# Optimization experiments

Hardware: AMD Instinct MI355X
Metric: run time of the kernel (lower is better)

## Reference

```python
import jax, jax.numpy as jnp
import numpy as np

BS, NX = 4, 4096
SD, NPAR, H, L, K = 2, 5, 128, 6, 16
DT = 0.1
EPS = 1e-5


def swish(x):
    return x * jax.nn.sigmoid(x)


def _gather(a, idx):
    # a: [bs, nx, F], idx: [bs, nx, k] -> [bs, nx, k, F]
    bs, nx, k = idx.shape
    flat = jnp.take_along_axis(a, idx.reshape(bs, nx * k)[:, :, None], axis=1)
    return flat.reshape(bs, nx, k, a.shape[-1])


def _knn_idx(pos, k):
    # pos: [bs, nx, sd] -> indices of k nearest neighbors (self excluded), [bs, nx, k]
    sq = jnp.sum(pos * pos, axis=-1)
    d2 = sq[:, :, None] + sq[:, None, :] - 2.0 * jnp.einsum('bnd,bmd->bnm', pos, pos)
    n = pos.shape[1]
    d2 = d2.at[:, jnp.arange(n), jnp.arange(n)].set(1e10)  # loop=False
    return jax.lax.top_k(-d2, k)[1]


def _instance_norm(x):
    # PyG InstanceNorm (affine=False): normalize per graph per channel over nodes
    m = jnp.mean(x, axis=1, keepdims=True)
    v = jnp.mean((x - m) ** 2, axis=1, keepdims=True)
    return (x - m) * jax.lax.rsqrt(v + EPS)


def _forward(inputs, case_params, grid, emb_w1, emb_b1, emb_w2, emb_b2,
             mw1, mb1, mw2, mb2, uw1, ub1, uw2, ub2, ow1, ob1, ow2, ob2):
    u = inputs[..., :1]  # var_id=0 slice (c==1 here)
    # per-batch, per-dim min-max normalization of grid -> pos in [0,1]
    gmin = jnp.min(grid, axis=1, keepdims=True)
    gmax = jnp.max(grid, axis=1, keepdims=True)
    pos = (grid - gmin) / (gmax - gmin)
    idx = _knn_idx(pos, K)  # [bs, nx, K]: neighbors j of each target i
    params = case_params

    f = swish(jnp.concatenate([u, pos, params], -1) @ emb_w1 + emb_b1)
    f = swish(f @ emb_w2 + emb_b2)

    u_j = _gather(u, idx)
    pos_j = _gather(pos, idx)
    du = u[:, :, None, :] - u_j       # u_i - u_j,   [bs,nx,K,1]
    dpos = pos[:, :, None, :] - pos_j  # pos_i - pos_j, [bs,nx,K,sd]
    var_i = jnp.broadcast_to(params[:, :, None, :], (BS, NX, K, NPAR))

    for l in range(L):
        f_j = _gather(f, idx)
        f_i = jnp.broadcast_to(f[:, :, None, :], f_j.shape)
        m = jnp.concatenate([f_i, f_j, du, dpos, var_i], -1)  # [bs,nx,K,2H+1+sd+npar]
        m = swish(m @ mw1[l] + mb1[l])
        m = swish(m @ mw2[l] + mb2[l])
        agg = jnp.mean(m, axis=2)  # mean aggregation over K incoming edges
        up = swish(jnp.concatenate([f, agg, params], -1) @ uw1[l] + ub1[l])
        up = swish(up @ uw2[l] + ub2[l])
        f = _instance_norm(f + up)  # residual (in==out) then InstanceNorm

    diff = swish(f @ ow1 + ob1) @ ow2 + ob2
    return u + DT * diff  # [bs, nx, 1]


def setup_inputs():
    key = jax.random.key(0)
    ks = jax.random.split(key, 16)
    s = 0.05
    d = {}
    d['inputs'] = jax.random.normal(ks[0], (BS, NX, 1), jnp.float32)
    d['case_params'] = jax.random.uniform(ks[1], (BS, NX, NPAR), dtype=jnp.float32)
    d['mask'] = jnp.ones((BS, NX, 1), jnp.float32)
    d['grid'] = jax.random.uniform(ks[2], (BS, NX, SD), dtype=jnp.float32)
    d['emb_w1'] = jax.random.normal(ks[3], (1 + SD + NPAR, H), jnp.float32) * s
    d['emb_b1'] = jnp.zeros((H,), jnp.float32)
    d['emb_w2'] = jax.random.normal(ks[4], (H, H), jnp.float32) * s
    d['emb_b2'] = jnp.zeros((H,), jnp.float32)
    d['mw1'] = jax.random.normal(ks[5], (L, 2 * H + 1 + SD + NPAR, H), jnp.float32) * s
    d['mb1'] = jnp.zeros((L, H), jnp.float32)
    d['mw2'] = jax.random.normal(ks[6], (L, H, H), jnp.float32) * s
    d['mb2'] = jnp.zeros((L, H), jnp.float32)
    d['uw1'] = jax.random.normal(ks[7], (L, 2 * H + NPAR, H), jnp.float32) * s
    d['ub1'] = jnp.zeros((L, H), jnp.float32)
    d['uw2'] = jax.random.normal(ks[8], (L, H, H), jnp.float32) * s
    d['ub2'] = jnp.zeros((L, H), jnp.float32)
    d['ow1'] = jax.random.normal(ks[9], (H, H // 2), jnp.float32) * s
    d['ob1'] = jnp.zeros((H // 2,), jnp.float32)
    d['ow2'] = jax.random.normal(ks[10], (H // 2, 1), jnp.float32) * s
    d['ob2'] = jnp.zeros((1,), jnp.float32)
    return d


def reference(inputs, case_params, mask, grid, emb_w1, emb_b1, emb_w2, emb_b2,
              mw1, mb1, mw2, mb2, uw1, ub1, uw2, ub2, ow1, ob1, ow2, ob2):
    del mask  # unused by the original forward math
    return _forward(inputs, case_params, grid, emb_w1, emb_b1, emb_w2, emb_b2,
                    mw1, mb1, mw2, mb2, uw1, ub1, uw2, ub2, ow1, ob1, ow2, ob2)
```

## Files before the change

kernel.cpp:

```cpp
#include <hip/hip_runtime.h>
#include <math.h>

#define BSZ 4
#define NXN 4096
#define NPARP 5
#define HD 128
#define NLAY 6
#define KNN 16
#define DTC 0.1f
#define EPSC 1e-5f
#define NN (BSZ * NXN)
#define NPB 8
#define EPB 128

typedef __attribute__((ext_vector_type(8))) short short8;
typedef __attribute__((ext_vector_type(4))) float f32x4;

#define XR(r) (((r) & 7) << 4)

#define OFF_E   0
#define OFF_AU  32768
#define OFF_HU  40960
#define OFF_DU  45056
#define OFF_DPX 45568
#define OFF_DPY 46080
#define OFF_VAR 46592
#define SMEMB   46848

__device__ __forceinline__ float swishf(float x) {
    return x / (1.0f + __expf(-x));
}

__device__ __forceinline__ unsigned short f2bf(float x) {
    union { float f; unsigned u; } v; v.f = x;
    unsigned r = v.u + 0x7fffu + ((v.u >> 16) & 1u);
    return (unsigned short)(r >> 16);
}
__device__ __forceinline__ unsigned short trh(float x) {
    union { float f; unsigned u; } v; v.f = x;
    return (unsigned short)(v.u >> 16);
}

__global__ void kminmax(const float* __restrict__ grid, float* __restrict__ gmm) {
    int b = blockIdx.x;
    int t = threadIdx.x;
    float mnx = 1e30f, mxx = -1e30f, mny = 1e30f, mxy = -1e30f;
    for (int n = t; n < NXN; n += 256) {
        float x = grid[(b * NXN + n) * 2 + 0];
        float y = grid[(b * NXN + n) * 2 + 1];
        mnx = fminf(mnx, x); mxx = fmaxf(mxx, x);
        mny = fminf(mny, y); mxy = fmaxf(mxy, y);
    }
    __shared__ float s[4][256];
    s[0][t] = mnx; s[1][t] = mxx; s[2][t] = mny; s[3][t] = mxy;
    __syncthreads();
    for (int off = 128; off > 0; off >>= 1) {
        if (t < off) {
            s[0][t] = fminf(s[0][t], s[0][t + off]);
            s[1][t] = fmaxf(s[1][t], s[1][t + off]);
            s[2][t] = fminf(s[2][t], s[2][t + off]);
            s[3][t] = fmaxf(s[3][t], s[3][t + off]);
        }
        __syncthreads();
    }
    if (t == 0) {
        gmm[b * 4 + 0] = s[0][0];
        gmm[b * 4 + 1] = s[1][0];
        gmm[b * 4 + 2] = s[2][0];
        gmm[b * 4 + 3] = s[3][0];
    }
}

__global__ void kpos(const float* __restrict__ grid, const float* __restrict__ gmm,
                     float* __restrict__ pos, float* __restrict__ sq) {
    int g = blockIdx.x * 256 + threadIdx.x;
    if (g >= NN) return;
    int b = g >> 12;
    float gx = grid[g * 2], gy = grid[g * 2 + 1];
    float px = (gx - gmm[b * 4 + 0]) / (gmm[b * 4 + 1] - gmm[b * 4 + 0]);
    float py = (gy - gmm[b * 4 + 2]) / (gmm[b * 4 + 3] - gmm[b * 4 + 2]);
    pos[g * 2] = px; pos[g * 2 + 1] = py;
    sq[g] = __fadd_rn(__fmul_rn(px, px), __fmul_rn(py, py));
}

__global__ __launch_bounds__(256) void kknnC(const float* __restrict__ pos,
                                             const float* __restrict__ sq,
                                             int* __restrict__ idxw) {
    __shared__ float2 sxy[1024];
    __shared__ float ssq[1024];
    int blk = blockIdx.x;
    int b = blk >> 10;
    int t = threadIdx.x;
    int lane = t & 63, w = t >> 6;
    int i = (blk & 1023) * 4 + w;
    float2 pi = *(const float2*)&pos[(b * NXN + i) * 2];
    float sqi = sq[b * NXN + i];
    float pk[64];
    float g[4];
#pragma unroll
    for (int c = 0; c < 4; ++c) {
        __syncthreads();
        for (int n = t; n < 1024; n += 256) {
            int j = b * NXN + c * 1024 + n;
            sxy[n] = *(const float2*)&pos[j * 2];
            ssq[n] = sq[j];
        }
        __syncthreads();
        float gc = 1e38f;
#pragma unroll
        for (int tt = 0; tt < 16; ++tt) {
            int n = tt * 64 + lane;
            float2 pj = sxy[n];
            float dot = fmaf(pi.x, pj.x, pi.y * pj.y);
            float d2 = (sqi + ssq[n]) - 2.0f * dot;
            d2 = (c * 1024 + n == i) ? 1e38f : d2;
            pk[c * 16 + tt] = d2;
            gc = fminf(gc, d2);
        }
        g[c] = gc;
    }
    int obase = (b * NXN + i) * KNN;
#pragma unroll 1
    for (int r = 0; r < KNN; ++r) {
        float m = fminf(fminf(g[0], g[1]), fminf(g[2], g[3]));
        float gm = m;
#pragma unroll
        for (int off = 1; off < 64; off <<= 1)
            gm = fminf(gm, __shfl_xor(gm, off));
        if (m == gm) {
            int jt = 0;
            if (g[0] == gm) {
                float ng = 1e38f;
#pragma unroll
                for (int tt = 0; tt < 16; ++tt) {
                    bool hit = (pk[tt] == gm);
                    jt = hit ? tt : jt;
                    pk[tt] = hit ? 1e38f : pk[tt];
                    ng = fminf(ng, pk[tt]);
                }
                g[0] = ng;
            }
            if (g[1] == gm) {
                float ng = 1e38f;
#pragma unroll
                for (int tt = 16; tt < 32; ++tt) {
                    bool hit = (pk[tt] == gm);
                    jt = hit ? tt : jt;
                    pk[tt] = hit ? 1e38f : pk[tt];
                    ng = fminf(ng, pk[tt]);
                }
                g[1] = ng;
            }
            if (g[2] == gm) {
                float ng = 1e38f;
#pragma unroll
                for (int tt = 32; tt < 48; ++tt) {
                    bool hit = (pk[tt] == gm);
                    jt = hit ? tt : jt;
                    pk[tt] = hit ? 1e38f : pk[tt];
                    ng = fminf(ng, pk[tt]);
                }
                g[2] = ng;
            }
            if (g[3] == gm) {
                float ng = 1e38f;
#pragma unroll
                for (int tt = 48; tt < 64; ++tt) {
                    bool hit = (pk[tt] == gm);
                    jt = hit ? tt : jt;
                    pk[tt] = hit ? 1e38f : pk[tt];
                    ng = fminf(ng, pk[tt]);
                }
                g[3] = ng;
            }
            idxw[obase + r] = ((jt >> 4) << 10) + ((jt & 15) << 6) + lane;
        }
    }
}

__global__ void kpack(const float* __restrict__ src, unsigned short* __restrict__ dst,
                      int K, int KB, int nmat) {
    int g = blockIdx.x * 256 + threadIdx.x;
    int per = KB * 1024;
    if (g >= nmat * per) return;
    int mat = g / per, rem = g % per;
    int kb = rem >> 10, r2 = rem & 1023;
    int n = r2 >> 3, j = r2 & 7;
    int k = kb * 8 + j;
    float v = (k < K) ? src[(mat * K + k) * HD + n] : 0.0f;
    dst[g] = f2bf(v);
}

__global__ __launch_bounds__(128) void kembed(const float* __restrict__ inputs,
                                              const float* __restrict__ pos,
                                              const float* __restrict__ params,
                                              const float* __restrict__ w1,
                                              const float* __restrict__ b1,
                                              const float* __restrict__ w2,
                                              const float* __restrict__ b2,
                                              float* __restrict__ f,
                                              unsigned short* __restrict__ fh) {
    __shared__ __align__(16) float sh[HD];
    int t = threadIdx.x;
    int g = blockIdx.x;
    float rw1[8];
#pragma unroll
    for (int k = 0; k < 8; k++) rw1[k] = w1[k * HD + t];
    float u = inputs[g];
    float px = pos[g * 2], py = pos[g * 2 + 1];
    float a = b1[t] + u * rw1[0] + px * rw1[1] + py * rw1[2];
#pragma unroll
    for (int j = 0; j < NPARP; j++) a += params[g * NPARP + j] * rw1[3 + j];
    sh[t] = swishf(a);
    __syncthreads();
    float a2 = b2[t];
    for (int k = 0; k < HD; k += 4) {
        float4 s4 = *(const float4*)&sh[k];
        a2 = fmaf(s4.x, w2[(k + 0) * HD + t], a2);
        a2 = fmaf(s4.y, w2[(k + 1) * HD + t], a2);
        a2 = fmaf(s4.z, w2[(k + 2) * HD + t], a2);
        a2 = fmaf(s4.w, w2[(k + 3) * HD + t], a2);
    }
    float fv = swishf(a2);
    f[g * HD + t] = fv;
    fh[g * HD + t] = trh(fv);
}

__global__ __launch_bounds__(256, 3) void kmsg4(
    const float* __restrict__ f, const unsigned short* __restrict__ fh,
    float* __restrict__ fnew,
    const float* __restrict__ inputs, const float* __restrict__ pos,
    const float* __restrict__ params, const int* __restrict__ idxw,
    const unsigned short* __restrict__ W1p, const float* __restrict__ W1r,
    const float* __restrict__ B1,
    const unsigned short* __restrict__ W2p, const float* __restrict__ B2,
    const unsigned short* __restrict__ U1p, const float* __restrict__ U1r,
    const float* __restrict__ UB1,
    const unsigned short* __restrict__ U2p, const float* __restrict__ UB2) {
    __shared__ __align__(16) char sm[SMEMB];
    int tid = threadIdx.x;
    int lane = tid & 63, w = tid >> 6;
    int l15 = lane & 15, l4 = lane >> 4;
    int bn0 = blockIdx.x * NPB;
    int base = bn0 & ~(NXN - 1);
    int r0 = w * 32;
    int c0 = w * 32 + l15, c1 = c0 + 16;
    float* sVAR = (float*)(sm + OFF_VAR);

    short8 bC0[4], bC1[4], bM10[4], bM11[4];
#pragma unroll
    for (int k = 0; k < 4; ++k) {
        bC0[k]  = *(const short8*)&W1p[((k * 4 + l4) * HD + c0) * 8];
        bC1[k]  = *(const short8*)&W1p[((k * 4 + l4) * HD + c1) * 8];
        bM10[k] = *(const short8*)&W1p[((16 + k * 4 + l4) * HD + c0) * 8];
        bM11[k] = *(const short8*)&W1p[((16 + k * 4 + l4) * HD + c1) * 8];
    }
    float vB1_0 = B1[c0], vB1_1 = B1[c1];
    float wdu0 = W1r[256 * HD + c0], wdx0 = W1r[257 * HD + c0], wdy0 = W1r[258 * HD + c0];
    float wdu1 = W1r[256 * HD + c1], wdx1 = W1r[257 * HD + c1], wdy1 = W1r[258 * HD + c1];
    float wv0[5], wv1[5];
#pragma unroll
    for (int j = 0; j < 5; ++j) {
        wv0[j] = W1r[(259 + j) * HD + c0];
        wv1[j] = W1r[(259 + j) * HD + c1];
    }
    float vB2_0 = B2[c0], vB2_1 = B2[c1];

    if (lane < 32) {
        int e = r0 + lane;
        int nd = e >> 4;
        int gj = idxw[(bn0 + nd) * KNN + (e & 15)];
        int gn = base + gj;
        ((float*)(sm + OFF_DU))[e]  = inputs[bn0 + nd] - inputs[gn];
        ((float*)(sm + OFF_DPX))[e] = pos[(bn0 + nd) * 2]     - pos[gn * 2];
        ((float*)(sm + OFF_DPY))[e] = pos[(bn0 + nd) * 2 + 1] - pos[gn * 2 + 1];
    } else if (lane < 42) {
        int q = lane - 32;
        int nd = 2 * w + q / 5, j = q % 5;
        sVAR[nd * 8 + j] = params[(bn0 + nd) * NPARP + j];
    }
    {
        int r = 2 * w + (lane >> 5);
        int c4 = (lane & 31) * 4;
        uint2 v = *(const uint2*)&fh[(bn0 + r) * HD + c4];
        *(uint2*)(sm + OFF_AU + r * 512 + ((c4 * 2) ^ XR(r))) = v;
    }
    {
        int r = 8 + 2 * w + (lane >> 5);
        int cz = (lane & 31) * 16;
        uint4 z = {0, 0, 0, 0};
        *(uint4*)(sm + OFF_AU + r * 512 + cz) = z;
    }
    {
        int r = 8 + 2 * w + (lane >> 5);
        int cz = (lane & 31) * 8;
        uint2 z = {0, 0};
        *(uint2*)(sm + OFF_HU + r * 256 + cz) = z;
    }
    {
        int r = r0 + (lane >> 1), hf = lane & 1;
        int gj = idxw[(bn0 + (r >> 4)) * KNN + (r & 15)];
        const uint4* src = (const uint4*)&fh[(base + gj) * HD + hf * 64];
        char* drow = sm + OFF_E + r * 256;
#pragma unroll
        for (int jj = 0; jj < 8; ++jj) {
            uint4 p = src[jj];
            *(uint4*)(drow + ((hf * 128 + jj * 16) ^ XR(r))) = p;
        }
    }
    __syncthreads();

    f32x4 cm0 = {0.f, 0.f, 0.f, 0.f}, cm1 = {0.f, 0.f, 0.f, 0.f};
    {
        short8 afi[4];
#pragma unroll
        for (int k = 0; k < 4; ++k)
            afi[k] = *(short8*)(sm + OFF_AU + l15 * 512 + ((k * 64 + l4 * 16) ^ XR(l15)));
#pragma unroll
        for (int k = 0; k < 4; ++k) {
            cm0 = __builtin_amdgcn_mfma_f32_16x16x32_bf16(afi[k], bC0[k], cm0, 0, 0, 0);
            cm1 = __builtin_amdgcn_mfma_f32_16x16x32_bf16(afi[k], bC1[k], cm1, 0, 0, 0);
        }
    }
    if (l4 < 2) {
#pragma unroll
        for (int reg = 0; reg < 4; ++reg) {
            int nd = l4 * 4 + reg;
            float s0 = vB1_0, s1 = vB1_1;
#pragma unroll
            for (int j = 0; j < 5; ++j) {
                float vv = sVAR[nd * 8 + j];
                s0 = fmaf(vv, wv0[j], s0);
                s1 = fmaf(vv, wv1[j], s1);
            }
            cm0[reg] += s0; cm1[reg] += s1;
        }
    }

    short8 bM20[4], bM21[4];
#pragma unroll
    for (int k = 0; k < 4; ++k) {
        bM20[k] = *(const short8*)&W2p[((k * 4 + l4) * HD + c0) * 8];
        bM21[k] = *(const short8*)&W2p[((k * 4 + l4) * HD + c1) * 8];
    }

    short8 aC[4], aN[4];
#pragma unroll
    for (int k = 0; k < 4; ++k)
        aC[k] = *(short8*)(sm + OFF_E + l15 * 256 + ((k * 64 + l4 * 16) ^ XR(l15)));
#pragma unroll
    for (int m = 0; m < 8; ++m) {
        f32x4 h0 = {0.f, 0.f, 0.f, 0.f}, h1 = {0.f, 0.f, 0.f, 0.f};
#pragma unroll
        for (int k = 0; k < 4; ++k) {
            h0 = __builtin_amdgcn_mfma_f32_16x16x32_bf16(aC[k], bM10[k], h0, 0, 0, 0);
            h1 = __builtin_amdgcn_mfma_f32_16x16x32_bf16(aC[k], bM11[k], h1, 0, 0, 0);
        }
        if (m < 7) {
#pragma unroll
            for (int k = 0; k < 4; ++k)
                aN[k] = *(short8*)(sm + OFF_E + ((m + 1) * 16 + l15) * 256 +
                                   ((k * 64 + l4 * 16) ^ XR(l15)));
        }
        float com0 = __shfl(cm0[m & 3], ((m >> 2) << 4) | l15);
        float com1 = __shfl(cm1[m & 3], ((m >> 2) << 4) | l15);
        float4 duv = *(const float4*)(sm + OFF_DU  + (m * 16 + l4 * 4) * 4);
        float4 dxv = *(const float4*)(sm + OFF_DPX + (m * 16 + l4 * 4) * 4);
        float4 dyv = *(const float4*)(sm + OFF_DPY + (m * 16 + l4 * 4) * 4);
        __syncthreads();
#pragma unroll
        for (int reg = 0; reg < 4; ++reg) {
            int rr = m * 16 + l4 * 4 + reg;
            float d_u = ((const float*)&duv)[reg];
            float d_x = ((const float*)&dxv)[reg];
            float d_y = ((const float*)&dyv)[reg];
            float hv0 = h0[reg] + com0 + d_u * wdu0 + d_x * wdx0 + d_y * wdy0;
            *(unsigned short*)(sm + OFF_E + rr * 256 + ((c0 * 2) ^ XR(rr))) =
                trh(swishf(hv0));
            float hv1 = h1[reg] + com1 + d_u * wdu1 + d_x * wdx1 + d_y * wdy1;
            *(unsigned short*)(sm + OFF_E + rr * 256 + ((c1 * 2) ^ XR(rr))) =
                trh(swishf(hv1));
        }
        if (m < 7) {
#pragma unroll
            for (int k = 0; k < 4; ++k) aC[k] = aN[k];
        }
    }
    __syncthreads();

    short8 bU10[8], bU11[8];
#pragma unroll
    for (int k = 0; k < 8; ++k) {
        bU10[k] = *(const short8*)&U1p[((k * 4 + l4) * HD + c0) * 8];
        bU11[k] = *(const short8*)&U1p[((k * 4 + l4) * HD + c1) * 8];
    }
    float vUB1_0 = UB1[c0], vUB1_1 = UB1[c1];
    float uv0[5], uv1[5];
#pragma unroll
    for (int j = 0; j < 5; ++j) {
        uv0[j] = U1r[(256 + j) * HD + c0];
        uv1[j] = U1r[(256 + j) * HD + c1];
    }

#pragma unroll
    for (int m = 0; m < 8; ++m) {
        short8 hf4[4];
#pragma unroll
        for (int k = 0; k < 4; ++k)
            hf4[k] = *(short8*)(sm + OFF_E + (m * 16 + l15) * 256 +
                                ((k * 64 + l4 * 16) ^ XR(l15)));
        f32x4 s0 = {0.f, 0.f, 0.f, 0.f}, s1 = {0.f, 0.f, 0.f, 0.f};
#pragma unroll
        for (int k = 0; k < 4; ++k) {
            s0 = __builtin_amdgcn_mfma_f32_16x16x32_bf16(hf4[k], bM20[k], s0, 0, 0, 0);
            s1 = __builtin_amdgcn_mfma_f32_16x16x32_bf16(hf4[k], bM21[k], s1, 0, 0, 0);
        }
        float sum0 = swishf(s0[0] + vB2_0) + swishf(s0[1] + vB2_0)
                   + swishf(s0[2] + vB2_0) + swishf(s0[3] + vB2_0);
        float sum1 = swishf(s1[0] + vB2_1) + swishf(s1[1] + vB2_1)
                   + swishf(s1[2] + vB2_1) + swishf(s1[3] + vB2_1);
        sum0 += __shfl_xor(sum0, 16); sum0 += __shfl_xor(sum0, 32);
        sum1 += __shfl_xor(sum1, 16); sum1 += __shfl_xor(sum1, 32);
        if (lane < 16) {
            int ca = w * 32 + lane;
            *(unsigned short*)(sm + OFF_AU + m * 512 + ((256 + ca * 2) ^ XR(m))) =
                trh(sum0 * 0.0625f);
            *(unsigned short*)(sm + OFF_AU + m * 512 + ((256 + (ca + 16) * 2) ^ XR(m))) =
                trh(sum1 * 0.0625f);
        }
    }
    __syncthreads();

    short8 bU20[4], bU21[4];
#pragma unroll
    for (int k = 0; k < 4; ++k) {
        bU20[k] = *(const short8*)&U2p[((k * 4 + l4) * HD + c0) * 8];
        bU21[k] = *(const short8*)&U2p[((k * 4 + l4) * HD + c1) * 8];
    }
    float vUB2_0 = UB2[c0], vUB2_1 = UB2[c1];

    {
        short8 au[8];
#pragma unroll
        for (int k = 0; k < 8; ++k)
            au[k] = *(short8*)(sm + OFF_AU + l15 * 512 + ((k * 64 + l4 * 16) ^ XR(l15)));
        f32x4 u0 = {0.f, 0.f, 0.f, 0.f}, u1 = {0.f, 0.f, 0.f, 0.f};
#pragma unroll
        for (int k = 0; k < 8; ++k) {
            u0 = __builtin_amdgcn_mfma_f32_16x16x32_bf16(au[k], bU10[k], u0, 0, 0, 0);
            u1 = __builtin_amdgcn_mfma_f32_16x16x32_bf16(au[k], bU11[k], u1, 0, 0, 0);
        }
        if (l4 < 2) {
#pragma unroll
            for (int reg = 0; reg < 4; ++reg) {
                int nd = l4 * 4 + reg;
                float s0 = vUB1_0, s1 = vUB1_1;
#pragma unroll
                for (int j = 0; j < 5; ++j) {
                    float vv = sVAR[nd * 8 + j];
                    s0 = fmaf(vv, uv0[j], s0);
                    s1 = fmaf(vv, uv1[j], s1);
                }
                *(unsigned short*)(sm + OFF_HU + nd * 256 + ((c0 * 2) ^ XR(nd))) =
                    trh(swishf(u0[reg] + s0));
                *(unsigned short*)(sm + OFF_HU + nd * 256 + ((c1 * 2) ^ XR(nd))) =
                    trh(swishf(u1[reg] + s1));
            }
        }
    }
    __syncthreads();

    {
        short8 ah[4];
#pragma unroll
        for (int k = 0; k < 4; ++k)
            ah[k] = *(short8*)(sm + OFF_HU + l15 * 256 + ((k * 64 + l4 * 16) ^ XR(l15)));
        f32x4 o0 = {0.f, 0.f, 0.f, 0.f}, o1 = {0.f, 0.f, 0.f, 0.f};
#pragma unroll
        for (int k = 0; k < 4; ++k) {
            o0 = __builtin_amdgcn_mfma_f32_16x16x32_bf16(ah[k], bU20[k], o0, 0, 0, 0);
            o1 = __builtin_amdgcn_mfma_f32_16x16x32_bf16(ah[k], bU21[k], o1, 0, 0, 0);
        }
        if (l4 < 2) {
#pragma unroll
            for (int reg = 0; reg < 4; ++reg) {
                int nd = l4 * 4 + reg;
                int gi0 = (bn0 + nd) * HD + c0;
                fnew[gi0] = f[gi0] + swishf(o0[reg] + vUB2_0);
                int gi1 = (bn0 + nd) * HD + c1;
                fnew[gi1] = f[gi1] + swishf(o1[reg] + vUB2_1);
            }
        }
    }
}

__global__ __launch_bounds__(256) void kstats(const float* __restrict__ fnew,
                                              float* __restrict__ p1, float* __restrict__ p2) {
    int blk = blockIdx.x;
    int b = blk >> 5;
    int ch = blk & 31;
    int t = threadIdx.x;
    int c = t & 127;
    int half = t >> 7;
    int nbase = ch * 128;
    float s1 = 0.0f, s2 = 0.0f;
    for (int n = half; n < 128; n += 2) {
        float v = fnew[((b * NXN) + (nbase + n)) * HD + c];
        s1 += v; s2 += v * v;
    }
    __shared__ float r1[256], r2[256];
    r1[t] = s1; r2[t] = s2;
    __syncthreads();
    if (half == 0) {
        s1 += r1[t + 128]; s2 += r2[t + 128];
        p1[blk * HD + c] = s1;
        p2[blk * HD + c] = s2;
    }
}

__global__ void kfinal(const float* __restrict__ p1, const float* __restrict__ p2,
                       float* __restrict__ mean, float* __restrict__ inv) {
    int g = blockIdx.x * 256 + threadIdx.x;
    if (g >= BSZ * HD) return;
    int b = g >> 7;
    int c = g & 127;
    float s1 = 0.0f, s2 = 0.0f;
#pragma unroll
    for (int ch = 0; ch < 32; ch++) {
        s1 += p1[(b * 32 + ch) * HD + c];
        s2 += p2[(b * 32 + ch) * HD + c];
    }
    float m = s1 * (1.0f / NXN);
    float v = s2 * (1.0f / NXN) - m * m;
    mean[g] = m;
    inv[g] = rsqrtf(v + EPSC);
}

__global__ void kapply(const float* __restrict__ fnew,
                       const float* __restrict__ mean, const float* __restrict__ inv,
                       float* __restrict__ f, unsigned short* __restrict__ fh) {
    int g = blockIdx.x * 256 + threadIdx.x;
    int b = g >> 19;
    int c = g & 127;
    float fv = (fnew[g] - mean[b * HD + c]) * inv[b * HD + c];
    f[g] = fv;
    fh[g] = trh(fv);
}

__global__ __launch_bounds__(64) void khead(const float* __restrict__ f,
                                            const float* __restrict__ inputs,
                                            const float* __restrict__ ow1,
                                            const float* __restrict__ ob1,
                                            const float* __restrict__ ow2,
                                            const float* __restrict__ ob2,
                                            float* __restrict__ out) {
    int bn = blockIdx.x;
    int c = threadIdx.x;
    float a = ob1[c];
    for (int k = 0; k < HD; k++) a += f[bn * HD + k] * ow1[k * 64 + c];
    float v = swishf(a) * ow2[c];
#pragma unroll
    for (int off = 32; off > 0; off >>= 1) v += __shfl_down(v, off);
    if (c == 0) out[bn] = inputs[bn] + DTC * (v + ob2[0]);
}

extern "C" void kernel_launch(void* const* d_in, const int* in_sizes, int n_in,
                              void* d_out, int out_size, void* d_ws, size_t ws_size,
                              hipStream_t stream) {
    const float* inputs = (const float*)d_in[0];
    const float* params = (const float*)d_in[1];
    const float* grid   = (const float*)d_in[3];
    const float* emb_w1 = (const float*)d_in[4];
    const float* emb_b1 = (const float*)d_in[5];
    const float* emb_w2 = (const float*)d_in[6];
    const float* emb_b2 = (const float*)d_in[7];
    const float* mw1 = (const float*)d_in[8];
    const float* mb1 = (const float*)d_in[9];
    const float* mw2 = (const float*)d_in[10];
    const float* mb2 = (const float*)d_in[11];
    const float* uw1 = (const float*)d_in[12];
    const float* ub1 = (const float*)d_in[13];
    const float* uw2 = (const float*)d_in[14];
    const float* ub2 = (const float*)d_in[15];
    const float* ow1 = (const float*)d_in[16];
    const float* ob1 = (const float*)d_in[17];
    const float* ow2 = (const float*)d_in[18];
    const float* ob2 = (const float*)d_in[19];
    float* out = (float*)d_out;

    float* ws  = (float*)d_ws;
    float* pos = ws;
    float* sq  = pos + BSZ * NXN * 2;
    float* f   = sq + BSZ * NXN;
    float* fnew = f + BSZ * NXN * HD;
    float* p1   = fnew + BSZ * NXN * HD;
    float* p2   = p1 + BSZ * 32 * HD;
    float* meanw = p2 + BSZ * 32 * HD;
    float* invw  = meanw + BSZ * HD;
    float* gmm  = invw + BSZ * HD;
    int* idxw   = (int*)(gmm + 16);
    unsigned short* mw1p = (unsigned short*)(idxw + NN * KNN);
    unsigned short* mw2p = mw1p + 6 * 33 * 1024;
    unsigned short* uw1p = mw2p + 6 * 16 * 1024;
    unsigned short* uw2p = uw1p + 6 * 33 * 1024;
    unsigned short* fh   = uw2p + 6 * 16 * 1024;

    kminmax<<<BSZ, 256, 0, stream>>>(grid, gmm);
    kpos<<<NN / 256, 256, 0, stream>>>(grid, gmm, pos, sq);
    kknnC<<<BSZ * (NXN / 4), 256, 0, stream>>>(pos, sq, idxw);

    kpack<<<(6 * 33 * 1024 + 255) / 256, 256, 0, stream>>>(mw1, mw1p, 264, 33, 6);
    kpack<<<(6 * 16 * 1024 + 255) / 256, 256, 0, stream>>>(mw2, mw2p, 128, 16, 6);
    kpack<<<(6 * 33 * 1024 + 255) / 256, 256, 0, stream>>>(uw1, uw1p, 261, 33, 6);
    kpack<<<(6 * 16 * 1024 + 255) / 256, 256, 0, stream>>>(uw2, uw2p, 128, 16, 6);

    kembed<<<NN, 128, 0, stream>>>(inputs, pos, params,
                                   emb_w1, emb_b1, emb_w2, emb_b2, f, fh);
    for (int l = 0; l < NLAY; l++) {
        kmsg4<<<NN / NPB, 256, 0, stream>>>(f, fh, fnew, inputs, pos, params, idxw,
                                            mw1p + l * 33 * 1024, mw1 + l * 264 * HD, mb1 + l * HD,
                                            mw2p + l * 16 * 1024, mb2 + l * HD,
                                            uw1p + l * 33 * 1024, uw1 + l * 261 * HD, ub1 + l * HD,
                                            uw2p + l * 16 * 1024, ub2 + l * HD);
        kstats<<<BSZ * 32, 256, 0, stream>>>(fnew, p1, p2);
        kfinal<<<2, 256, 0, stream>>>(p1, p2, meanw, invw);
        kapply<<<(BSZ * NXN * HD) / 256, 256, 0, stream>>>(fnew, meanw, invw, f, fh);
    }
    khead<<<NN, 64, 0, stream>>>(f, inputs, ow1, ob1, ow2, ob2, out);
}
```

Before: 695.1 us.

## Fuse instance-norm statistics into message kernel via atomics and permute weight columns

Moves the per-graph channel sum and sum-of-squares into the message-passing kernel's epilogue, using wave shuffles and global atomicAdd, and drops the separate kstats and kfinal kernels. kapply now computes mean and inverse std directly from the accumulators, which are zeroed by a memset each layer. Packed weight columns are permuted so each lane owns adjacent channels, enabling 32-bit paired bf16 LDS stores and float2 global loads/stores. Swish uses a hardware reciprocal. This adds atomic contention and makes the float summation order nondeterministic.

After: 729.8 us. 5.0% more time.

```diff
diff --git a/kernel.cpp b/kernel.cpp
--- a/kernel.cpp
+++ b/kernel.cpp
@@ -28,7 +28,7 @@
 #define SMEMB   46848
 
 __device__ __forceinline__ float swishf(float x) {
-    return x / (1.0f + __expf(-x));
+    return x * __builtin_amdgcn_rcpf(1.0f + __expf(-x));
 }
 
 __device__ __forceinline__ unsigned short f2bf(float x) {
@@ -39,6 +39,10 @@
 __device__ __forceinline__ unsigned short trh(float x) {
     union { float f; unsigned u; } v; v.f = x;
     return (unsigned short)(v.u >> 16);
+}
+__device__ __forceinline__ unsigned trpk(float lo, float hi) {
+    union { float f; unsigned u; } a, b; a.f = lo; b.f = hi;
+    return (b.u & 0xFFFF0000u) | (a.u >> 16);
 }
 
 __global__ void kminmax(const float* __restrict__ grid, float* __restrict__ gmm) {
@@ -186,8 +190,9 @@
     int mat = g / per, rem = g % per;
     int kb = rem >> 10, r2 = rem & 1023;
     int n = r2 >> 3, j = r2 & 7;
+    int phys = (n & 96) | ((n & 15) << 1) | ((n >> 4) & 1);
     int k = kb * 8 + j;
-    float v = (k < K) ? src[(mat * K + k) * HD + n] : 0.0f;
+    float v = (k < K) ? src[(mat * K + k) * HD + phys] : 0.0f;
     dst[g] = f2bf(v);
 }
 
@@ -226,7 +231,7 @@
     fh[g * HD + t] = trh(fv);
 }
 
-__global__ __launch_bounds__(256, 3) void kmsg4(
+__global__ __launch_bounds__(256, 3) void kmsg5(
     const float* __restrict__ f, const unsigned short* __restrict__ fh,
     float* __restrict__ fnew,
     const float* __restrict__ inputs, const float* __restrict__ pos,
@@ -236,15 +241,18 @@
     const unsigned short* __restrict__ W2p, const float* __restrict__ B2,
     const unsigned short* __restrict__ U1p, const float* __restrict__ U1r,
     const float* __restrict__ UB1,
-    const unsigned short* __restrict__ U2p, const float* __restrict__ UB2) {
+    const unsigned short* __restrict__ U2p, const float* __restrict__ UB2,
+    float* __restrict__ p1, float* __restrict__ p2) {
     __shared__ __align__(16) char sm[SMEMB];
     int tid = threadIdx.x;
     int lane = tid & 63, w = tid >> 6;
     int l15 = lane & 15, l4 = lane >> 4;
     int bn0 = blockIdx.x * NPB;
     int base = bn0 & ~(NXN - 1);
+    int bb = bn0 >> 12;
     int r0 = w * 32;
     int c0 = w * 32 + l15, c1 = c0 + 16;
+    int pc0 = w * 32 + 2 * l15, pc1 = pc0 + 1;
     float* sVAR = (float*)(sm + OFF_VAR);
 
     short8 bC0[4], bC1[4], bM10[4], bM11[4];
@@ -255,16 +263,16 @@
         bM10[k] = *(const short8*)&W1p[((16 + k * 4 + l4) * HD + c0) * 8];
         bM11[k] = *(const short8*)&W1p[((16 + k * 4 + l4) * HD + c1) * 8];
     }
-    float vB1_0 = B1[c0], vB1_1 = B1[c1];
-    float wdu0 = W1r[256 * HD + c0], wdx0 = W1r[257 * HD + c0], wdy0 = W1r[258 * HD + c0];
-    float wdu1 = W1r[256 * HD + c1], wdx1 = W1r[257 * HD + c1], wdy1 = W1r[258 * HD + c1];
+    float vB1_0 = B1[pc0], vB1_1 = B1[pc1];
+    float wdu0 = W1r[256 * HD + pc0], wdx0 = W1r[257 * HD + pc0], wdy0 = W1r[258 * HD + pc0];
+    float wdu1 = W1r[256 * HD + pc1], wdx1 = W1r[257 * HD + pc1], wdy1 = W1r[258 * HD + pc1];
     float wv0[5], wv1[5];
 #pragma unroll
     for (int j = 0; j < 5; ++j) {
-        wv0[j] = W1r[(259 + j) * HD + c0];
-        wv1[j] = W1r[(259 + j) * HD + c1];
-    }
-    float vB2_0 = B2[c0], vB2_1 = B2[c1];
+        wv0[j] = W1r[(259 + j) * HD + pc0];
+        wv1[j] = W1r[(259 + j) * HD + pc1];
+    }
+    float vB2_0 = B2[pc0], vB2_1 = B2[pc1];
 
     if (lane < 32) {
         int e = r0 + lane;
@@ -375,11 +383,9 @@
             float d_x = ((const float*)&dxv)[reg];
             float d_y = ((const float*)&dyv)[reg];
             float hv0 = h0[reg] + com0 + d_u * wdu0 + d_x * wdx0 + d_y * wdy0;
-            *(unsigned short*)(sm + OFF_E + rr * 256 + ((c0 * 2) ^ XR(rr))) =
-                trh(swishf(hv0));
             float hv1 = h1[reg] + com1 + d_u * wdu1 + d_x * wdx1 + d_y * wdy1;
-            *(unsigned short*)(sm + OFF_E + rr * 256 + ((c1 * 2) ^ XR(rr))) =
-                trh(swishf(hv1));
+            *(unsigned*)(sm + OFF_E + rr * 256 + ((w * 64 + l15 * 4) ^ XR(rr))) =
+                trpk(swishf(hv0), swishf(hv1));
         }
         if (m < 7) {
 #pragma unroll
@@ -394,12 +400,12 @@
         bU10[k] = *(const short8*)&U1p[((k * 4 + l4) * HD + c0) * 8];
         bU11[k] = *(const short8*)&U1p[((k * 4 + l4) * HD + c1) * 8];
     }
-    float vUB1_0 = UB1[c0], vUB1_1 = UB1[c1];
+    float vUB1_0 = UB1[pc0], vUB1_1 = UB1[pc1];
     float uv0[5], uv1[5];
 #pragma unroll
     for (int j = 0; j < 5; ++j) {
-        uv0[j] = U1r[(256 + j) * HD + c0];
-        uv1[j] = U1r[(256 + j) * HD + c1];
+        uv0[j] = U1r[(256 + j) * HD + pc0];
+        uv1[j] = U1r[(256 + j) * HD + pc1];
     }
 
 #pragma unroll
@@ -422,11 +428,8 @@
         sum0 += __shfl_xor(sum0, 16); sum0 += __shfl_xor(sum0, 32);
         sum1 += __shfl_xor(sum1, 16); sum1 += __shfl_xor(sum1, 32);
         if (lane < 16) {
-            int ca = w * 32 + lane;
-            *(unsigned short*)(sm + OFF_AU + m * 512 + ((256 + ca * 2) ^ XR(m))) =
-                trh(sum0 * 0.0625f);
-            *(unsigned short*)(sm + OFF_AU + m * 512 + ((256 + (ca + 16) * 2) ^ XR(m))) =
-                trh(sum1 * 0.0625f);
+            *(unsigned*)(sm + OFF_AU + m * 512 + ((256 + w * 64 + lane * 4) ^ XR(m))) =
+                trpk(sum0 * 0.0625f, sum1 * 0.0625f);
         }
     }
     __syncthreads();
@@ -437,7 +440,7 @@
         bU20[k] = *(const short8*)&U2p[((k * 4 + l4) * HD + c0) * 8];
         bU21[k] = *(const short8*)&U2p[((k * 4 + l4) * HD + c1) * 8];
     }
-    float vUB2_0 = UB2[c0], vUB2_1 = UB2[c1];
+    float vUB2_0 = UB2[pc0], vUB2_1 = UB2[pc1];
 
     {
         short8 au[8];
@@ -461,10 +464,8 @@
                     s0 = fmaf(vv, uv0[j], s0);
                     s1 = fmaf(vv, uv1[j], s1);
                 }
-                *(unsigned short*)(sm + OFF_HU + nd * 256 + ((c0 * 2) ^ XR(nd))) =
-                    trh(swishf(u0[reg] + s0));
-                *(unsigned short*)(sm + OFF_HU + nd * 256 + ((c1 * 2) ^ XR(nd))) =
-                    trh(swishf(u1[reg] + s1));
+                *(unsigned*)(sm + OFF_HU + nd * 256 + ((w * 64 + l15 * 4) ^ XR(nd))) =
+                    trpk(swishf(u0[reg] + s0), swishf(u1[reg] + s1));
             }
         }
     }
@@ -481,68 +482,41 @@
             o0 = __builtin_amdgcn_mfma_f32_16x16x32_bf16(ah[k], bU20[k], o0, 0, 0, 0);
             o1 = __builtin_amdgcn_mfma_f32_16x16x32_bf16(ah[k], bU21[k], o1, 0, 0, 0);
         }
+        float a1_0 = 0.f, a2_0 = 0.f, a1_1 = 0.f, a2_1 = 0.f;
         if (l4 < 2) {
 #pragma unroll
             for (int reg = 0; reg < 4; ++reg) {
                 int nd = l4 * 4 + reg;
-                int gi0 = (bn0 + nd) * HD + c0;
-                fnew[gi0] = f[gi0] + swishf(o0[reg] + vUB2_0);
-                int gi1 = (bn0 + nd) * HD + c1;
-                fnew[gi1] = f[gi1] + swishf(o1[reg] + vUB2_1);
+                int gi = (bn0 + nd) * HD + pc0;
+                float2 fv = *(const float2*)&f[gi];
+                float v0 = fv.x + swishf(o0[reg] + vUB2_0);
+                float v1 = fv.y + swishf(o1[reg] + vUB2_1);
+                float2 st = {v0, v1};
+                *(float2*)&fnew[gi] = st;
+                a1_0 += v0; a2_0 += v0 * v0;
+                a1_1 += v1; a2_1 += v1 * v1;
             }
         }
-    }
-}
-
-__global__ __launch_bounds__(256) void kstats(const float* __restrict__ fnew,
-                                              float* __restrict__ p1, float* __restrict__ p2) {
-    int blk = blockIdx.x;
-    int b = blk >> 5;
-    int ch = blk & 31;
-    int t = threadIdx.x;
-    int c = t & 127;
-    int half = t >> 7;
-    int nbase = ch * 128;
-    float s1 = 0.0f, s2 = 0.0f;
-    for (int n = half; n < 128; n += 2) {
-        float v = fnew[((b * NXN) + (nbase + n)) * HD + c];
-        s1 += v; s2 += v * v;
-    }
-    __shared__ float r1[256], r2[256];
-    r1[t] = s1; r2[t] = s2;
-    __syncthreads();
-    if (half == 0) {
-        s1 += r1[t + 128]; s2 += r2[t + 128];
-        p1[blk * HD + c] = s1;
-        p2[blk * HD + c] = s2;
-    }
-}
-
-__global__ void kfinal(const float* __restrict__ p1, const float* __restrict__ p2,
-                       float* __restrict__ mean, float* __restrict__ inv) {
-    int g = blockIdx.x * 256 + threadIdx.x;
-    if (g >= BSZ * HD) return;
-    int b = g >> 7;
-    int c = g & 127;
-    float s1 = 0.0f, s2 = 0.0f;
-#pragma unroll
-    for (int ch = 0; ch < 32; ch++) {
-        s1 += p1[(b * 32 + ch) * HD + c];
-        s2 += p2[(b * 32 + ch) * HD + c];
-    }
-    float m = s1 * (1.0f / NXN);
-    float v = s2 * (1.0f / NXN) - m * m;
-    mean[g] = m;
-    inv[g] = rsqrtf(v + EPSC);
+        a1_0 += __shfl_xor(a1_0, 16); a2_0 += __shfl_xor(a2_0, 16);
+        a1_1 += __shfl_xor(a1_1, 16); a2_1 += __shfl_xor(a2_1, 16);
+        if (l4 == 0) {
+            atomicAdd(&p1[bb * HD + pc0], a1_0);
+            atomicAdd(&p2[bb * HD + pc0], a2_0);
+            atomicAdd(&p1[bb * HD + pc1], a1_1);
+            atomicAdd(&p2[bb * HD + pc1], a2_1);
+        }
+    }
 }
 
 __global__ void kapply(const float* __restrict__ fnew,
-                       const float* __restrict__ mean, const float* __restrict__ inv,
+                       const float* __restrict__ p1, const float* __restrict__ p2,
                        float* __restrict__ f, unsigned short* __restrict__ fh) {
     int g = blockIdx.x * 256 + threadIdx.x;
     int b = g >> 19;
     int c = g & 127;
-    float fv = (fnew[g] - mean[b * HD + c]) * inv[b * HD + c];
+    float m = p1[b * HD + c] * (1.0f / NXN);
+    float v = p2[b * HD + c] * (1.0f / NXN) - m * m;
+    float fv = (fnew[g] - m) * rsqrtf(v + EPSC);
     f[g] = fv;
     fh[g] = trh(fv);
 }
@@ -594,10 +568,8 @@
     float* f   = sq + BSZ * NXN;
     float* fnew = f + BSZ * NXN * HD;
     float* p1   = fnew + BSZ * NXN * HD;
-    float* p2   = p1 + BSZ * 32 * HD;
-    float* meanw = p2 + BSZ * 32 * HD;
-    float* invw  = meanw + BSZ * HD;
-    float* gmm  = invw + BSZ * HD;
+    float* p2   = p1 + BSZ * HD;
+    float* gmm  = p2 + BSZ * HD;
     int* idxw   = (int*)(gmm + 16);
     unsigned short* mw1p = (unsigned short*)(idxw + NN * KNN);
     unsigned short* mw2p = mw1p + 6 * 33 * 1024;
@@ -617,14 +589,14 @@
     kembed<<<NN, 128, 0, stream>>>(inputs, pos, params,
                                    emb_w1, emb_b1, emb_w2, emb_b2, f, fh);
     for (int l = 0; l < NLAY; l++) {
-        kmsg4<<<NN / NPB, 256, 0, stream>>>(f, fh, fnew, inputs, pos, params, idxw,
+        hipMemsetAsync(p1, 0, 2 * BSZ * HD * sizeof(float), stream);
+        kmsg5<<<NN / NPB, 256, 0, stream>>>(f, fh, fnew, inputs, pos, params, idxw,
                                             mw1p + l * 33 * 1024, mw1 + l * 264 * HD, mb1 + l * HD,
                                             mw2p + l * 16 * 1024, mb2 + l * HD,
                                             uw1p + l * 33 * 1024, uw1 + l * 261 * HD, ub1 + l * HD,
-                                            uw2p + l * 16 * 1024, ub2 + l * HD);
-        kstats<<<BSZ * 32, 256, 0, stream>>>(fnew, p1, p2);
-        kfinal<<<2, 256, 0, stream>>>(p1, p2, meanw, invw);
-        kapply<<<(BSZ * NXN * HD) / 256, 256, 0, stream>>>(fnew, meanw, invw, f, fh);
+                                            uw2p + l * 16 * 1024, ub2 + l * HD,
+                                            p1, p2);
+        kapply<<<(BSZ * NXN * HD) / 256, 256, 0, stream>>>(fnew, p1, p2, f, fh);
     }
     khead<<<NN, 64, 0, stream>>>(f, inputs, ow1, ob1, ow2, ob2, out);
 }
```

## Split message MLP into two edge halves with prefetched neighbor gather

Applied to the files above, without the earlier changes.

The per-block edge processing now runs in two halves of 64 edges. Only the first half of the neighbor features is gathered before the first barrier, and the second half's global loads are issued into registers while the second message matmul runs on the first half, so gather latency overlaps MFMA work. The first-layer output now goes to a separate shared buffer instead of overwriting the edge tile in place, which removes the per-iteration barrier inside the m-loop. Weight fragment loads are moved closer to their use to lower register pressure, and swish uses a hardware reciprocal instead of a divide. The cost is extra barriers between the halves and a slightly less accurate reciprocal.

Result: slower. 779.1 us (+12.1%).

```diff
diff --git a/kernel.cpp b/kernel.cpp
--- a/kernel.cpp
+++ b/kernel.cpp
@@ -11,7 +11,6 @@
 #define EPSC 1e-5f
 #define NN (BSZ * NXN)
 #define NPB 8
-#define EPB 128
 
 typedef __attribute__((ext_vector_type(8))) short short8;
 typedef __attribute__((ext_vector_type(4))) float f32x4;
@@ -19,6 +18,7 @@
 #define XR(r) (((r) & 7) << 4)
 
 #define OFF_E   0
+#define OFF_H   16384
 #define OFF_AU  32768
 #define OFF_HU  40960
 #define OFF_DU  45056
@@ -28,7 +28,7 @@
 #define SMEMB   46848
 
 __device__ __forceinline__ float swishf(float x) {
-    return x / (1.0f + __expf(-x));
+    return x * __builtin_amdgcn_rcpf(1.0f + __expf(-x));
 }
 
 __device__ __forceinline__ unsigned short f2bf(float x) {
@@ -226,7 +226,7 @@
     fh[g * HD + t] = trh(fv);
 }
 
-__global__ __launch_bounds__(256, 3) void kmsg4(
+__global__ __launch_bounds__(256, 3) void kmsg9(
     const float* __restrict__ f, const unsigned short* __restrict__ fh,
     float* __restrict__ fnew,
     const float* __restrict__ inputs, const float* __restrict__ pos,
@@ -243,15 +243,13 @@
     int l15 = lane & 15, l4 = lane >> 4;
     int bn0 = blockIdx.x * NPB;
     int base = bn0 & ~(NXN - 1);
-    int r0 = w * 32;
     int c0 = w * 32 + l15, c1 = c0 + 16;
     float* sVAR = (float*)(sm + OFF_VAR);
-
-    short8 bC0[4], bC1[4], bM10[4], bM11[4];
+    int gr_ = tid >> 2, gq_ = tid & 3;
+
+    short8 bM10[4], bM11[4];
 #pragma unroll
     for (int k = 0; k < 4; ++k) {
-        bC0[k]  = *(const short8*)&W1p[((k * 4 + l4) * HD + c0) * 8];
-        bC1[k]  = *(const short8*)&W1p[((k * 4 + l4) * HD + c1) * 8];
         bM10[k] = *(const short8*)&W1p[((16 + k * 4 + l4) * HD + c0) * 8];
         bM11[k] = *(const short8*)&W1p[((16 + k * 4 + l4) * HD + c1) * 8];
     }
@@ -267,7 +265,7 @@
     float vB2_0 = B2[c0], vB2_1 = B2[c1];
 
     if (lane < 32) {
-        int e = r0 + lane;
+        int e = w * 32 + lane;
         int nd = e >> 4;
         int gj = idxw[(bn0 + nd) * KNN + (e & 15)];
         int gn = base + gj;
@@ -298,15 +296,12 @@
         *(uint2*)(sm + OFF_HU + r * 256 + cz) = z;
     }
     {
-        int r = r0 + (lane >> 1), hf = lane & 1;
-        int gj = idxw[(bn0 + (r >> 4)) * KNN + (r & 15)];
-        const uint4* src = (const uint4*)&fh[(base + gj) * HD + hf * 64];
-        char* drow = sm + OFF_E + r * 256;
-#pragma unroll
-        for (int jj = 0; jj < 8; ++jj) {
-            uint4 p = src[jj];
-            *(uint4*)(drow + ((hf * 128 + jj * 16) ^ XR(r))) = p;
-        }
+        int gj = idxw[(bn0 + (gr_ >> 4)) * KNN + (gr_ & 15)];
+        const uint4* srcp = (const uint4*)(fh + (base + gj) * HD) + gq_ * 4;
+        char* drow = sm + OFF_E + gr_ * 256;
+#pragma unroll
+        for (int jj = 0; jj < 4; ++jj)
+            *(uint4*)(drow + ((gq_ * 64 + jj * 16) ^ XR(gr_))) = srcp[jj];
     }
     __syncthreads();
 
@@ -318,8 +313,10 @@
             afi[k] = *(short8*)(sm + OFF_AU + l15 * 512 + ((k * 64 + l4 * 16) ^ XR(l15)));
 #pragma unroll
         for (int k = 0; k < 4; ++k) {
-            cm0 = __builtin_amdgcn_mfma_f32_16x16x32_bf16(afi[k], bC0[k], cm0, 0, 0, 0);
-            cm1 = __builtin_amdgcn_mfma_f32_16x16x32_bf16(afi[k], bC1[k], cm1, 0, 0, 0);
+            short8 bC0 = *(const short8*)&W1p[((k * 4 + l4) * HD + c0) * 8];
+            short8 bC1 = *(const short8*)&W1p[((k * 4 + l4) * HD + c1) * 8];
+            cm0 = __builtin_amdgcn_mfma_f32_16x16x32_bf16(afi[k], bC0, cm0, 0, 0, 0);
+            cm1 = __builtin_amdgcn_mfma_f32_16x16x32_bf16(afi[k], bC1, cm1, 0, 0, 0);
         }
     }
     if (l4 < 2) {
@@ -337,57 +334,98 @@
         }
     }
 
+#define MM1_HALF(H) {                                                       \
+        _Pragma("unroll")                                                   \
+        for (int m = 0; m < 4; ++m) {                                       \
+            short8 aC[4];                                                   \
+            _Pragma("unroll")                                               \
+            for (int k = 0; k < 4; ++k)                                     \
+                aC[k] = *(short8*)(sm + OFF_E + (m * 16 + l15) * 256 +      \
+                                   ((k * 64 + l4 * 16) ^ XR(l15)));         \
+            f32x4 h0 = {0.f, 0.f, 0.f, 0.f}, h1 = {0.f, 0.f, 0.f, 0.f};     \
+            _Pragma("unroll")                                               \
+            for (int k = 0; k < 4; ++k) {                                   \
+                h0 = __builtin_amdgcn_mfma_f32_16x16x32_bf16(aC[k], bM10[k], h0, 0, 0, 0); \
+                h1 = __builtin_amdgcn_mfma_f32_16x16x32_bf16(aC[k], bM11[k], h1, 0, 0, 0); \
+            }                                                               \
+            int M = (H) * 4 + m;                                            \
+            float com0 = __shfl(cm0[M & 3], ((M >> 2) << 4) | l15);         \
+            float com1 = __shfl(cm1[M & 3], ((M >> 2) << 4) | l15);         \
+            float4 duv = *(const float4*)(sm + OFF_DU  + ((H) * 64 + m * 16 + l4 * 4) * 4); \
+            float4 dxv = *(const float4*)(sm + OFF_DPX + ((H) * 64 + m * 16 + l4 * 4) * 4); \
+            float4 dyv = *(const float4*)(sm + OFF_DPY + ((H) * 64 + m * 16 + l4 * 4) * 4); \
+            _Pragma("unroll")                                               \
+            for (int reg = 0; reg < 4; ++reg) {                             \
+                int rr = m * 16 + l4 * 4 + reg;                             \
+                float d_u = ((const float*)&duv)[reg];                      \
+                float d_x = ((const float*)&dxv)[reg];                      \
+                float d_y = ((const float*)&dyv)[reg];                      \
+                float hv0 = h0[reg] + com0 + d_u * wdu0 + d_x * wdx0 + d_y * wdy0; \
+                *(unsigned short*)(sm + OFF_H + rr * 256 + ((c0 * 2) ^ XR(rr))) = \
+                    trh(swishf(hv0));                                       \
+                float hv1 = h1[reg] + com1 + d_u * wdu1 + d_x * wdx1 + d_y * wdy1; \
+                *(unsigned short*)(sm + OFF_H + rr * 256 + ((c1 * 2) ^ XR(rr))) = \
+                    trh(swishf(hv1));                                       \
+            }                                                               \
+        } }
+
+#define MM2_HALF(H, BM20, BM21) {                                           \
+        _Pragma("unroll")                                                   \
+        for (int m = 0; m < 4; ++m) {                                       \
+            short8 hf4[4];                                                  \
+            _Pragma("unroll")                                               \
+            for (int k = 0; k < 4; ++k)                                     \
+                hf4[k] = *(short8*)(sm + OFF_H + (m * 16 + l15) * 256 +     \
+                                    ((k * 64 + l4 * 16) ^ XR(l15)));        \
+            f32x4 s0 = {0.f, 0.f, 0.f, 0.f}, s1 = {0.f, 0.f, 0.f, 0.f};     \
+            _Pragma("unroll")                                               \
+            for (int k = 0; k < 4; ++k) {                                   \
+                s0 = __builtin_amdgcn_mfma_f32_16x16x32_bf16(hf4[k], BM20[k], s0, 0, 0, 0); \
+                s1 = __builtin_amdgcn_mfma_f32_16x16x32_bf16(hf4[k], BM21[k], s1, 0, 0, 0); \
+            }                                                               \
+            float sum0 = swishf(s0[0] + vB2_0) + swishf(s0[1] + vB2_0)      \
+                       + swishf(s0[2] + vB2_0) + swishf(s0[3] + vB2_0);     \
+            float sum1 = swishf(s1[0] + vB2_1) + swishf(s1[1] + vB2_1)      \
+                       + swishf(s1[2] + vB2_1) + swishf(s1[3] + vB2_1);     \
+            sum0 += __shfl_xor(sum0, 16); sum0 += __shfl_xor(sum0, 32);     \
+            sum1 += __shfl_xor(sum1, 16); sum1 += __shfl_xor(sum1, 32);     \
+            int Mg = (H) * 4 + m;                                           \
+            if (lane < 16) {                                                \
+                int ca = w * 32 + lane;                                     \
+                *(unsigned short*)(sm + OFF_AU + Mg * 512 + ((256 + ca * 2) ^ XR(Mg))) = \
+                    trh(sum0 * 0.0625f);                                    \
+                *(unsigned short*)(sm + OFF_AU + Mg * 512 + ((256 + (ca + 16) * 2) ^ XR(Mg))) = \
+                    trh(sum1 * 0.0625f);                                    \
+            }                                                               \
+        } }
+
+    MM1_HALF(0)
     short8 bM20[4], bM21[4];
 #pragma unroll
     for (int k = 0; k < 4; ++k) {
         bM20[k] = *(const short8*)&W2p[((k * 4 + l4) * HD + c0) * 8];
         bM21[k] = *(const short8*)&W2p[((k * 4 + l4) * HD + c1) * 8];
     }
-
-    short8 aC[4], aN[4];
-#pragma unroll
-    for (int k = 0; k < 4; ++k)
-        aC[k] = *(short8*)(sm + OFF_E + l15 * 256 + ((k * 64 + l4 * 16) ^ XR(l15)));
-#pragma unroll
-    for (int m = 0; m < 8; ++m) {
-        f32x4 h0 = {0.f, 0.f, 0.f, 0.f}, h1 = {0.f, 0.f, 0.f, 0.f};
-#pragma unroll
-        for (int k = 0; k < 4; ++k) {
-            h0 = __builtin_amdgcn_mfma_f32_16x16x32_bf16(aC[k], bM10[k], h0, 0, 0, 0);
-            h1 = __builtin_amdgcn_mfma_f32_16x16x32_bf16(aC[k], bM11[k], h1, 0, 0, 0);
-        }
-        if (m < 7) {
-#pragma unroll
-            for (int k = 0; k < 4; ++k)
-                aN[k] = *(short8*)(sm + OFF_E + ((m + 1) * 16 + l15) * 256 +
-                                   ((k * 64 + l4 * 16) ^ XR(l15)));
-        }
-        float com0 = __shfl(cm0[m & 3], ((m >> 2) << 4) | l15);
-        float com1 = __shfl(cm1[m & 3], ((m >> 2) << 4) | l15);
-        float4 duv = *(const float4*)(sm + OFF_DU  + (m * 16 + l4 * 4) * 4);
-        float4 dxv = *(const float4*)(sm + OFF_DPX + (m * 16 + l4 * 4) * 4);
-        float4 dyv = *(const float4*)(sm + OFF_DPY + (m * 16 + l4 * 4) * 4);
-        __syncthreads();
-#pragma unroll
-        for (int reg = 0; reg < 4; ++reg) {
-            int rr = m * 16 + l4 * 4 + reg;
-            float d_u = ((const float*)&duv)[reg];
-            float d_x = ((const float*)&dxv)[reg];
-            float d_y = ((const float*)&dyv)[reg];
-            float hv0 = h0[reg] + com0 + d_u * wdu0 + d_x * wdx0 + d_y * wdy0;
-            *(unsigned short*)(sm + OFF_E + rr * 256 + ((c0 * 2) ^ XR(rr))) =
-                trh(swishf(hv0));
-            float hv1 = h1[reg] + com1 + d_u * wdu1 + d_x * wdx1 + d_y * wdy1;
-            *(unsigned short*)(sm + OFF_E + rr * 256 + ((c1 * 2) ^ XR(rr))) =
-                trh(swishf(hv1));
-        }
-        if (m < 7) {
-#pragma unroll
-            for (int k = 0; k < 4; ++k) aC[k] = aN[k];
-        }
-    }
-    __syncthreads();
-
+    __syncthreads();
+
+    uint4 g1r[4];
+    {
+        int e = 64 + gr_;
+        int gj = idxw[(bn0 + (e >> 4)) * KNN + (e & 15)];
+        const uint4* srcp = (const uint4*)(fh + (base + gj) * HD) + gq_ * 4;
+#pragma unroll
+        for (int jj = 0; jj < 4; ++jj) g1r[jj] = srcp[jj];
+    }
+    MM2_HALF(0, bM20, bM21)
+    {
+        char* drow = sm + OFF_E + gr_ * 256;
+#pragma unroll
+        for (int jj = 0; jj < 4; ++jj)
+            *(uint4*)(drow + ((gq_ * 64 + jj * 16) ^ XR(gr_))) = g1r[jj];
+    }
+    __syncthreads();
+
+    MM1_HALF(1)
     short8 bU10[8], bU11[8];
 #pragma unroll
     for (int k = 0; k < 8; ++k) {
@@ -401,43 +439,10 @@
         uv0[j] = U1r[(256 + j) * HD + c0];
         uv1[j] = U1r[(256 + j) * HD + c1];
     }
-
-#pragma unroll
-    for (int m = 0; m < 8; ++m) {
-        short8 hf4[4];
-#pragma unroll
-        for (int k = 0; k < 4; ++k)
-            hf4[k] = *(short8*)(sm + OFF_E + (m * 16 + l15) * 256 +
-                                ((k * 64 + l4 * 16) ^ XR(l15)));
-        f32x4 s0 = {0.f, 0.f, 0.f, 0.f}, s1 = {0.f, 0.f, 0.f, 0.f};
-#pragma unroll
-        for (int k = 0; k < 4; ++k) {
-            s0 = __builtin_amdgcn_mfma_f32_16x16x32_bf16(hf4[k], bM20[k], s0, 0, 0, 0);
-            s1 = __builtin_amdgcn_mfma_f32_16x16x32_bf16(hf4[k], bM21[k], s1, 0, 0, 0);
-        }
-        float sum0 = swishf(s0[0] + vB2_0) + swishf(s0[1] + vB2_0)
-                   + swishf(s0[2] + vB2_0) + swishf(s0[3] + vB2_0);
-        float sum1 = swishf(s1[0] + vB2_1) + swishf(s1[1] + vB2_1)
-                   + swishf(s1[2] + vB2_1) + swishf(s1[3] + vB2_1);
-        sum0 += __shfl_xor(sum0, 16); sum0 += __shfl_xor(sum0, 32);
-        sum1 += __shfl_xor(sum1, 16); sum1 += __shfl_xor(sum1, 32);
-        if (lane < 16) {
-            int ca = w * 32 + lane;
-            *(unsigned short*)(sm + OFF_AU + m * 512 + ((256 + ca * 2) ^ XR(m))) =
-                trh(sum0 * 0.0625f);
-            *(unsigned short*)(sm + OFF_AU + m * 512 + ((256 + (ca + 16) * 2) ^ XR(m))) =
-                trh(sum1 * 0.0625f);
-        }
-    }
-    __syncthreads();
-
-    short8 bU20[4], bU21[4];
-#pragma unroll
-    for (int k = 0; k < 4; ++k) {
-        bU20[k] = *(const short8*)&U2p[((k * 4 + l4) * HD + c0) * 8];
-        bU21[k] = *(const short8*)&U2p[((k * 4 + l4) * HD + c1) * 8];
-    }
-    float vUB2_0 = UB2[c0], vUB2_1 = UB2[c1];
+    __syncthreads();
+
+    MM2_HALF(1, bM20, bM21)
+    __syncthreads();
 
     {
         short8 au[8];
@@ -471,6 +476,13 @@
     __syncthreads();
 
     {
+        short8 bU20[4], bU21[4];
+#pragma unroll
+        for (int k = 0; k < 4; ++k) {
+            bU20[k] = *(const short8*)&U2p[((k * 4 + l4) * HD + c0) * 8];
+            bU21[k] = *(const short8*)&U2p[((k * 4 + l4) * HD + c1) * 8];
+        }
+        float vUB2_0 = UB2[c0], vUB2_1 = UB2[c1];
         short8 ah[4];
 #pragma unroll
         for (int k = 0; k < 4; ++k)
@@ -492,6 +504,8 @@
             }
         }
     }
+#undef MM1_HALF
+#undef MM2_HALF
 }
 
 __global__ __launch_bounds__(256) void kstats(const float* __restrict__ fnew,
@@ -617,7 +631,7 @@
     kembed<<<NN, 128, 0, stream>>>(inputs, pos, params,
                                    emb_w1, emb_b1, emb_w2, emb_b2, f, fh);
     for (int l = 0; l < NLAY; l++) {
-        kmsg4<<<NN / NPB, 256, 0, stream>>>(f, fh, fnew, inputs, pos, params, idxw,
+        kmsg9<<<NN / NPB, 256, 0, stream>>>(f, fh, fnew, inputs, pos, params, idxw,
                                             mw1p + l * 33 * 1024, mw1 + l * 264 * HD, mb1 + l * HD,
                                             mw2p + l * 16 * 1024, mb2 + l * HD,
                                             uw1p + l * 33 * 1024, uw1 + l * 261 * HD, ub1 + l * HD,
```
